# Performance work log

Measured on AMD Instinct MI355X. Metric: run time of the kernel, lower is better.

## Reference

```python
import jax, jax.numpy as jnp
import numpy as np

N_CODES = 1024
DIM = 64
COMMITMENT = 0.25


def setup_inputs() -> dict:
    key = jax.random.key(0)
    k1, k2 = jax.random.split(key)
    z = jax.random.normal(k1, (32, DIM, 64, 64), dtype=jnp.float32)
    # nn.Embedding weight initialized uniform(-1/n_codes, 1/n_codes)
    codebook = jax.random.uniform(
        k2, (N_CODES, DIM), dtype=jnp.float32,
        minval=-1.0 / N_CODES, maxval=1.0 / N_CODES)
    return {"z": z, "codebook": codebook}


def reference(z, codebook):
    B, C, H, W = z.shape
    # (B,C,H,W) -> (B*H*W, C)
    z_flat = jnp.transpose(z, (0, 2, 3, 1)).reshape(-1, C)
    # squared L2 distances via expansion: |z|^2 + |e|^2 - 2 z.e
    dists = (
        jnp.sum(z_flat ** 2, axis=1, keepdims=True)
        + jnp.sum(codebook ** 2, axis=1)
        - 2.0 * z_flat @ codebook.T
    )  # [N, n_codes]
    indices = jnp.argmin(dists, axis=1)  # [N]
    z_q = jnp.transpose(codebook[indices].reshape(B, H, W, C), (0, 3, 1, 2))
    commit_loss = jnp.mean((jax.lax.stop_gradient(z_q) - z) ** 2)
    codebook_loss = jnp.mean((z_q - jax.lax.stop_gradient(z)) ** 2)
    vq_loss = codebook_loss + COMMITMENT * commit_loss
    z_q_st = z + jax.lax.stop_gradient(z_q - z)  # straight-through
    return (z_q_st, vq_loss)
```

## Files before the change

kernel.cpp:

```cpp
#include <hip/hip_runtime.h>


constexpr int DIM    = 64;
constexpr int NCODES = 1024;
constexpr int HWSZ   = 4096;
constexpr int NPOS   = 131072;
constexpr int BLOCK  = 1024;
constexpr int PPB    = 256;
constexpr int GRID   = NPOS / PPB;

typedef float    f32x4  __attribute__((ext_vector_type(4)));
typedef float    f32x2  __attribute__((ext_vector_type(2)));
typedef unsigned uint2v __attribute__((ext_vector_type(2)));
typedef unsigned uint4v __attribute__((ext_vector_type(4)));

__global__ __launch_bounds__(256) void vq_prep(const float* __restrict__ cb,
                                               float* __restrict__ cinitT,
                                               unsigned* __restrict__ cbq) {
    int j = blockIdx.x * 256 + threadIdx.x;
    const float4* src = (const float4*)(cb + (size_t)j * DIM);
    unsigned words[16];
    float nq = 0.f;
#pragma unroll
    for (int g8 = 0; g8 < 8; g8++) {
        float4 v0 = src[g8 * 2], v1 = src[g8 * 2 + 1];
        int lo = 0, hi = 0;
        lo = __builtin_amdgcn_cvt_pk_fp8_f32(v0.x * 512.f, v0.y * 512.f, lo, 0);
        lo = __builtin_amdgcn_cvt_pk_fp8_f32(v0.z * 512.f, v0.w * 512.f, lo, 1);
        hi = __builtin_amdgcn_cvt_pk_fp8_f32(v1.x * 512.f, v1.y * 512.f, hi, 0);
        hi = __builtin_amdgcn_cvt_pk_fp8_f32(v1.z * 512.f, v1.w * 512.f, hi, 1);
        words[g8 * 2] = (unsigned)lo; words[g8 * 2 + 1] = (unsigned)hi;
#pragma unroll
        for (int m = 0; m < 2; m++) {
            int wv = m ? hi : lo;
            f32x2 d0 = __builtin_amdgcn_cvt_pk_f32_fp8(wv, 0);
            f32x2 d1 = __builtin_amdgcn_cvt_pk_f32_fp8(wv, 1);
            nq += d0[0] * d0[0] + d0[1] * d0[1] + d1[0] * d1[0] + d1[1] * d1[1];
        }
    }
#pragma unroll
    for (int u = 0; u < 4; u++) {
        int us = u ^ (j & 3);
        uint4v t = {words[2 * u], words[2 * u + 1],
                    words[2 * u + 8], words[2 * u + 9]};
        *(uint4v*)(cbq + (size_t)j * 16 + us * 4) = t;
    }
    cinitT[(j & 15) * 64 + (j >> 4)] = 8.f - nq * (1.f / 1024.f);
}

__global__ __launch_bounds__(BLOCK, 8) void vq_main(const float* __restrict__ z,
                                                    const float* __restrict__ cinitT,
                                                    const unsigned* __restrict__ cbq,
                                                    float* __restrict__ out,
                                                    float* __restrict__ wsblk) {
    __shared__ __align__(16) unsigned char cb_lds[NCODES * DIM];
    __shared__ int   bj_lds[PPB];
    __shared__ float ls_lds[BLOCK / 64];

    const int tid  = threadIdx.x;
    const int w    = tid >> 6;
    const int lane = tid & 63;
    const int q    = lane >> 4;
    const int r    = lane & 15;
    const int p0   = blockIdx.x * PPB;
    const int b    = p0 >> 12;
    const int hwb  = p0 & 4095;

#pragma unroll
    for (int it = 0; it < (NCODES * DIM) / (BLOCK * 16); it++) {
        int off = (it * BLOCK + tid) * 16;
        __builtin_amdgcn_global_load_lds(
            (const __attribute__((address_space(1))) void*)((const char*)cbq + off),
            (__attribute__((address_space(3))) void*)(cb_lds + off), 16, 0, 0);
    }

    long  afrag[2];
    float zsq;
    {
        const float* zb = z + (size_t)b * DIM * HWSZ + hwb + w * 16 + r;
        float sq = 0.f;
#pragma unroll
        for (int h = 0; h < 2; h++) {
            float v[8];
#pragma unroll
            for (int i = 0; i < 8; i++) {
                v[i] = zb[(size_t)(h * 32 + q * 8 + i) * HWSZ];
                sq = fmaf(v[i], v[i], sq);
            }
            int lo = 0, hi = 0;
            lo = __builtin_amdgcn_cvt_pk_fp8_f32(v[0], v[1], lo, 0);
            lo = __builtin_amdgcn_cvt_pk_fp8_f32(v[2], v[3], lo, 1);
            hi = __builtin_amdgcn_cvt_pk_fp8_f32(v[4], v[5], hi, 0);
            hi = __builtin_amdgcn_cvt_pk_fp8_f32(v[6], v[7], hi, 1);
            uint2v u = {(unsigned)lo, (unsigned)hi};
            afrag[h] = __builtin_bit_cast(long, u);
        }
        sq += __shfl_xor(sq, 16, 64);
        sq += __shfl_xor(sq, 32, 64);
        zsq = sq;
    }

    __syncthreads();

    const int bbase = r * 64 + ((q ^ (r & 3)) * 16);

    float best[4];
#pragma unroll
    for (int g = 0; g < 4; g++) best[g] = 0.f;
    float tmp[4];

    uint4v Bp[2];
    Bp[0] = *(const uint4v*)&cb_lds[0 * 1024 + bbase];
    Bp[1] = *(const uint4v*)&cb_lds[1 * 1024 + bbase];
    float4 ci[2];
    ci[0] = *(const float4*)(cinitT + r * 64 + 0);
    ci[1] = *(const float4*)(cinitT + r * 64 + 4);

#pragma unroll
    for (int G = 0; G < 16; G++) {
#pragma unroll
        for (int e = 0; e < 4; e++) {
            const int jt   = G * 4 + e;
            const int slot = jt & 1;
            const int row  = jt * 16;
            const float cin = ci[G & 1][e];
            const unsigned inv_j = (unsigned)(1023 - row);
            uint2v blo = {Bp[slot][0], Bp[slot][1]};
            uint2v bhi = {Bp[slot][2], Bp[slot][3]};
            f32x4 c0 = {cin, cin, cin, cin};
            f32x4 acc = __builtin_amdgcn_mfma_f32_16x16x32_fp8_fp8(
                afrag[0], __builtin_bit_cast(long, blo), c0, 0, 0, 0);
            acc = __builtin_amdgcn_mfma_f32_16x16x32_fp8_fp8(
                afrag[1], __builtin_bit_cast(long, bhi), acc, 0, 0, 0);
#pragma unroll
            for (int g = 0; g < 4; g++) {
                unsigned bits = (__float_as_uint(acc[g]) & ~1023u)
                              | (inv_j - (unsigned)r);
                float pf = __uint_as_float(bits);
                if ((jt & 1) == 0) {
                    tmp[g] = pf;
                } else {
                    best[g] = fmaxf(fmaxf(best[g], tmp[g]), pf);
                }
            }
            Bp[slot] = *(const uint4v*)&cb_lds[(((jt + 2) & 63) * 1024) + bbase];
        }
        ci[G & 1] = *(const float4*)(cinitT + r * 64 + (((G + 2) & 15) * 4));
    }

    unsigned bestu[4];
#pragma unroll
    for (int g = 0; g < 4; g++) {
        unsigned v = __float_as_uint(best[g]);
#pragma unroll
        for (int off = 1; off < 16; off <<= 1) {
            unsigned v2 = __shfl_xor((int)v, off, 64);
            v = v > v2 ? v : v2;
        }
        bestu[g] = v;
    }

    float lsum = 0.f;
    if (q == (r >> 2)) {
        int g = r & 3;
        unsigned v = bestu[0];
        v = (g == 1) ? bestu[1] : v;
        v = (g == 2) ? bestu[2] : v;
        v = (g == 3) ? bestu[3] : v;
        bj_lds[w * 16 + r] = 1023 - (int)(v & 1023u);
        lsum = zsq + (8.f - __uint_as_float(v)) * (1.f / 256.f);
    }
#pragma unroll
    for (int off = 32; off > 0; off >>= 1) lsum += __shfl_down(lsum, off, 64);
    if (lane == 0) ls_lds[w] = lsum;
    __syncthreads();
    if (tid == 0) {
        float s = 0.f;
#pragma unroll
        for (int i = 0; i < BLOCK / 64; i++) s += ls_lds[i];
        wsblk[blockIdx.x] = s;
    }

    int posi = tid & 255;
    int u    = tid >> 8;
    int myj  = bj_lds[posi];
    int us   = u ^ (myj & 3);
    uint4v t = *(const uint4v*)&cb_lds[(size_t)myj * 64 + us * 16];
    float* ob = out + (size_t)b * DIM * HWSZ + hwb + posi;
#pragma unroll
    for (int m = 0; m < 2; m++) {
        int cbase = (m == 0) ? (8 * u) : (32 + 8 * u);
#pragma unroll
        for (int wd = 0; wd < 2; wd++) {
            int word = (int)t[m * 2 + wd];
            f32x2 d0 = __builtin_amdgcn_cvt_pk_f32_fp8(word, 0);
            f32x2 d1 = __builtin_amdgcn_cvt_pk_f32_fp8(word, 1);
            ob[(size_t)(cbase + wd * 4 + 0) * HWSZ] = d0[0] * (1.f / 512.f);
            ob[(size_t)(cbase + wd * 4 + 1) * HWSZ] = d0[1] * (1.f / 512.f);
            ob[(size_t)(cbase + wd * 4 + 2) * HWSZ] = d1[0] * (1.f / 512.f);
            ob[(size_t)(cbase + wd * 4 + 3) * HWSZ] = d1[1] * (1.f / 512.f);
        }
    }
}

__global__ void vq_fin(const float* __restrict__ wsblk, float* __restrict__ out_loss) {
    int t = threadIdx.x;
    float s = 0.f;
#pragma unroll
    for (int k = 0; k < GRID / 64; k++) s += wsblk[t + k * 64];
#pragma unroll
    for (int off = 32; off > 0; off >>= 1) s += __shfl_down(s, off, 64);
    if (t == 0) out_loss[0] = 1.25f * s / (float)((size_t)NPOS * DIM);
}

extern "C" void kernel_launch(void* const* d_in, const int* in_sizes, int n_in,
                              void* d_out, int out_size, void* d_ws, size_t ws_size,
                              hipStream_t stream) {
    const float* z  = (const float*)d_in[0];
    const float* cb = (const float*)d_in[1];
    float* out = (float*)d_out;

    float*    cinitT = (float*)d_ws;
    unsigned* cbq    = (unsigned*)((char*)d_ws + 4096);
    float*    wsblk  = (float*)((char*)d_ws + 4096 + 65536);

    vq_prep<<<NCODES / 256, 256, 0, stream>>>(cb, cinitT, cbq);
    vq_main<<<GRID, BLOCK, 0, stream>>>(z, cinitT, cbq, out, wsblk);
    vq_fin<<<1, 64, 0, stream>>>(wsblk, out + (size_t)NPOS * DIM);
}
```

Measured before the change: 106.3 us.

## Split z quantization into a separate pre-pass kernel writing packed fp8 fragments

Moves the fp32 z read, fp8 packing and |z|^2 partial sums out of the main search kernel into a new full-grid vq_quant kernel, which also absorbs the codebook prep on its first four blocks. The main kernel then loads one 16-byte packed fragment per lane instead of 16 strided fp32 loads, so the LDS-occupying, MFMA-bound kernel spends less time waiting on global memory. In exchange it adds a full extra launch and an 8 MB intermediate write and read. It also relies on codebook prep finishing before vq_main, which stream ordering guarantees.

After: 109.0 us. +2.5%, slower.

```diff
diff --git a/kernel.cpp b/kernel.cpp
--- a/kernel.cpp
+++ b/kernel.cpp
@@ -14,49 +14,13 @@
 typedef unsigned uint2v __attribute__((ext_vector_type(2)));
 typedef unsigned uint4v __attribute__((ext_vector_type(4)));
 
-__global__ __launch_bounds__(256) void vq_prep(const float* __restrict__ cb,
-                                               float* __restrict__ cinitT,
-                                               unsigned* __restrict__ cbq) {
-    int j = blockIdx.x * 256 + threadIdx.x;
-    const float4* src = (const float4*)(cb + (size_t)j * DIM);
-    unsigned words[16];
-    float nq = 0.f;
-#pragma unroll
-    for (int g8 = 0; g8 < 8; g8++) {
-        float4 v0 = src[g8 * 2], v1 = src[g8 * 2 + 1];
-        int lo = 0, hi = 0;
-        lo = __builtin_amdgcn_cvt_pk_fp8_f32(v0.x * 512.f, v0.y * 512.f, lo, 0);
-        lo = __builtin_amdgcn_cvt_pk_fp8_f32(v0.z * 512.f, v0.w * 512.f, lo, 1);
-        hi = __builtin_amdgcn_cvt_pk_fp8_f32(v1.x * 512.f, v1.y * 512.f, hi, 0);
-        hi = __builtin_amdgcn_cvt_pk_fp8_f32(v1.z * 512.f, v1.w * 512.f, hi, 1);
-        words[g8 * 2] = (unsigned)lo; words[g8 * 2 + 1] = (unsigned)hi;
-#pragma unroll
-        for (int m = 0; m < 2; m++) {
-            int wv = m ? hi : lo;
-            f32x2 d0 = __builtin_amdgcn_cvt_pk_f32_fp8(wv, 0);
-            f32x2 d1 = __builtin_amdgcn_cvt_pk_f32_fp8(wv, 1);
-            nq += d0[0] * d0[0] + d0[1] * d0[1] + d1[0] * d1[0] + d1[1] * d1[1];
-        }
-    }
-#pragma unroll
-    for (int u = 0; u < 4; u++) {
-        int us = u ^ (j & 3);
-        uint4v t = {words[2 * u], words[2 * u + 1],
-                    words[2 * u + 8], words[2 * u + 9]};
-        *(uint4v*)(cbq + (size_t)j * 16 + us * 4) = t;
-    }
-    cinitT[(j & 15) * 64 + (j >> 4)] = 8.f - nq * (1.f / 1024.f);
-}
-
-__global__ __launch_bounds__(BLOCK, 8) void vq_main(const float* __restrict__ z,
-                                                    const float* __restrict__ cinitT,
-                                                    const unsigned* __restrict__ cbq,
-                                                    float* __restrict__ out,
-                                                    float* __restrict__ wsblk) {
-    __shared__ __align__(16) unsigned char cb_lds[NCODES * DIM];
-    __shared__ int   bj_lds[PPB];
+__global__ __launch_bounds__(BLOCK, 8) void vq_quant(const float* __restrict__ z,
+                                                     const float* __restrict__ cb,
+                                                     float* __restrict__ cinitT,
+                                                     unsigned* __restrict__ cbq,
+                                                     unsigned* __restrict__ zq,
+                                                     float* __restrict__ zs) {
     __shared__ float ls_lds[BLOCK / 64];
-
     const int tid  = threadIdx.x;
     const int w    = tid >> 6;
     const int lane = tid & 63;
@@ -66,6 +30,89 @@
     const int b    = p0 >> 12;
     const int hwb  = p0 & 4095;
 
+    const float* zb = z + (size_t)b * DIM * HWSZ + hwb + w * 16 + r;
+    float sq = 0.f;
+    unsigned wd[4];
+#pragma unroll
+    for (int h = 0; h < 2; h++) {
+        float v[8];
+#pragma unroll
+        for (int i = 0; i < 8; i++) {
+            v[i] = zb[(size_t)(h * 32 + q * 8 + i) * HWSZ];
+            sq = fmaf(v[i], v[i], sq);
+        }
+        int lo = 0, hi = 0;
+        lo = __builtin_amdgcn_cvt_pk_fp8_f32(v[0], v[1], lo, 0);
+        lo = __builtin_amdgcn_cvt_pk_fp8_f32(v[2], v[3], lo, 1);
+        hi = __builtin_amdgcn_cvt_pk_fp8_f32(v[4], v[5], hi, 0);
+        hi = __builtin_amdgcn_cvt_pk_fp8_f32(v[6], v[7], hi, 1);
+        wd[h * 2] = (unsigned)lo; wd[h * 2 + 1] = (unsigned)hi;
+    }
+    uint4v av = {wd[0], wd[1], wd[2], wd[3]};
+    *(uint4v*)(zq + ((size_t)(blockIdx.x * 16 + w) * 64 + lane) * 4) = av;
+
+#pragma unroll
+    for (int off = 32; off > 0; off >>= 1) sq += __shfl_down(sq, off, 64);
+    if (lane == 0) ls_lds[w] = sq;
+    __syncthreads();
+    if (tid == 0) {
+        float s = 0.f;
+#pragma unroll
+        for (int i = 0; i < BLOCK / 64; i++) s += ls_lds[i];
+        zs[blockIdx.x] = s;
+    }
+
+    if (blockIdx.x < 4 && tid < 256) {
+        int j = blockIdx.x * 256 + tid;
+        const float4* src = (const float4*)(cb + (size_t)j * DIM);
+        unsigned words[16];
+        float nq = 0.f;
+#pragma unroll
+        for (int g8 = 0; g8 < 8; g8++) {
+            float4 v0 = src[g8 * 2], v1 = src[g8 * 2 + 1];
+            int lo = 0, hi = 0;
+            lo = __builtin_amdgcn_cvt_pk_fp8_f32(v0.x * 512.f, v0.y * 512.f, lo, 0);
+            lo = __builtin_amdgcn_cvt_pk_fp8_f32(v0.z * 512.f, v0.w * 512.f, lo, 1);
+            hi = __builtin_amdgcn_cvt_pk_fp8_f32(v1.x * 512.f, v1.y * 512.f, hi, 0);
+            hi = __builtin_amdgcn_cvt_pk_fp8_f32(v1.z * 512.f, v1.w * 512.f, hi, 1);
+            words[g8 * 2] = (unsigned)lo; words[g8 * 2 + 1] = (unsigned)hi;
+#pragma unroll
+            for (int m = 0; m < 2; m++) {
+                int wv = m ? hi : lo;
+                f32x2 d0 = __builtin_amdgcn_cvt_pk_f32_fp8(wv, 0);
+                f32x2 d1 = __builtin_amdgcn_cvt_pk_f32_fp8(wv, 1);
+                nq += d0[0] * d0[0] + d0[1] * d0[1] + d1[0] * d1[0] + d1[1] * d1[1];
+            }
+        }
+#pragma unroll
+        for (int u = 0; u < 4; u++) {
+            int us = u ^ (j & 3);
+            uint4v t = {words[2 * u], words[2 * u + 1],
+                        words[2 * u + 8], words[2 * u + 9]};
+            *(uint4v*)(cbq + (size_t)j * 16 + us * 4) = t;
+        }
+        cinitT[(j & 15) * 64 + (j >> 4)] = 8.f - nq * (1.f / 1024.f);
+    }
+}
+
+__global__ __launch_bounds__(BLOCK, 8) void vq_main(const unsigned* __restrict__ zq,
+                                                    const float* __restrict__ cinitT,
+                                                    const unsigned* __restrict__ cbq,
+                                                    float* __restrict__ out,
+                                                    float* __restrict__ sc) {
+    __shared__ __align__(16) unsigned char cb_lds[NCODES * DIM];
+    __shared__ int   bj_lds[PPB];
+    __shared__ float ls_lds[BLOCK / 64];
+
+    const int tid  = threadIdx.x;
+    const int w    = tid >> 6;
+    const int lane = tid & 63;
+    const int q    = lane >> 4;
+    const int r    = lane & 15;
+    const int p0   = blockIdx.x * PPB;
+    const int b    = p0 >> 12;
+    const int hwb  = p0 & 4095;
+
 #pragma unroll
     for (int it = 0; it < (NCODES * DIM) / (BLOCK * 16); it++) {
         int off = (it * BLOCK + tid) * 16;
@@ -74,31 +121,10 @@
             (__attribute__((address_space(3))) void*)(cb_lds + off), 16, 0, 0);
     }
 
-    long  afrag[2];
-    float zsq;
-    {
-        const float* zb = z + (size_t)b * DIM * HWSZ + hwb + w * 16 + r;
-        float sq = 0.f;
-#pragma unroll
-        for (int h = 0; h < 2; h++) {
-            float v[8];
-#pragma unroll
-            for (int i = 0; i < 8; i++) {
-                v[i] = zb[(size_t)(h * 32 + q * 8 + i) * HWSZ];
-                sq = fmaf(v[i], v[i], sq);
-            }
-            int lo = 0, hi = 0;
-            lo = __builtin_amdgcn_cvt_pk_fp8_f32(v[0], v[1], lo, 0);
-            lo = __builtin_amdgcn_cvt_pk_fp8_f32(v[2], v[3], lo, 1);
-            hi = __builtin_amdgcn_cvt_pk_fp8_f32(v[4], v[5], hi, 0);
-            hi = __builtin_amdgcn_cvt_pk_fp8_f32(v[6], v[7], hi, 1);
-            uint2v u = {(unsigned)lo, (unsigned)hi};
-            afrag[h] = __builtin_bit_cast(long, u);
-        }
-        sq += __shfl_xor(sq, 16, 64);
-        sq += __shfl_xor(sq, 32, 64);
-        zsq = sq;
-    }
+    uint4v av = *(const uint4v*)(zq + ((size_t)(blockIdx.x * 16 + w) * 64 + lane) * 4);
+    uint2v a0 = {av[0], av[1]}, a1 = {av[2], av[3]};
+    const long afrag0 = __builtin_bit_cast(long, a0);
+    const long afrag1 = __builtin_bit_cast(long, a1);
 
     __syncthreads();
 
@@ -129,9 +155,9 @@
             uint2v bhi = {Bp[slot][2], Bp[slot][3]};
             f32x4 c0 = {cin, cin, cin, cin};
             f32x4 acc = __builtin_amdgcn_mfma_f32_16x16x32_fp8_fp8(
-                afrag[0], __builtin_bit_cast(long, blo), c0, 0, 0, 0);
+                afrag0, __builtin_bit_cast(long, blo), c0, 0, 0, 0);
             acc = __builtin_amdgcn_mfma_f32_16x16x32_fp8_fp8(
-                afrag[1], __builtin_bit_cast(long, bhi), acc, 0, 0, 0);
+                afrag1, __builtin_bit_cast(long, bhi), acc, 0, 0, 0);
 #pragma unroll
             for (int g = 0; g < 4; g++) {
                 unsigned bits = (__float_as_uint(acc[g]) & ~1023u)
@@ -168,7 +194,7 @@
         v = (g == 2) ? bestu[2] : v;
         v = (g == 3) ? bestu[3] : v;
         bj_lds[w * 16 + r] = 1023 - (int)(v & 1023u);
-        lsum = zsq + (8.f - __uint_as_float(v)) * (1.f / 256.f);
+        lsum = (8.f - __uint_as_float(v)) * (1.f / 256.f);
     }
 #pragma unroll
     for (int off = 32; off > 0; off >>= 1) lsum += __shfl_down(lsum, off, 64);
@@ -178,7 +204,7 @@
         float s = 0.f;
 #pragma unroll
         for (int i = 0; i < BLOCK / 64; i++) s += ls_lds[i];
-        wsblk[blockIdx.x] = s;
+        sc[blockIdx.x] = s;
     }
 
     int posi = tid & 255;
@@ -191,23 +217,24 @@
     for (int m = 0; m < 2; m++) {
         int cbase = (m == 0) ? (8 * u) : (32 + 8 * u);
 #pragma unroll
-        for (int wd = 0; wd < 2; wd++) {
-            int word = (int)t[m * 2 + wd];
+        for (int wdx = 0; wdx < 2; wdx++) {
+            int word = (int)t[m * 2 + wdx];
             f32x2 d0 = __builtin_amdgcn_cvt_pk_f32_fp8(word, 0);
             f32x2 d1 = __builtin_amdgcn_cvt_pk_f32_fp8(word, 1);
-            ob[(size_t)(cbase + wd * 4 + 0) * HWSZ] = d0[0] * (1.f / 512.f);
-            ob[(size_t)(cbase + wd * 4 + 1) * HWSZ] = d0[1] * (1.f / 512.f);
-            ob[(size_t)(cbase + wd * 4 + 2) * HWSZ] = d1[0] * (1.f / 512.f);
-            ob[(size_t)(cbase + wd * 4 + 3) * HWSZ] = d1[1] * (1.f / 512.f);
-        }
-    }
-}
-
-__global__ void vq_fin(const float* __restrict__ wsblk, float* __restrict__ out_loss) {
+            ob[(size_t)(cbase + wdx * 4 + 0) * HWSZ] = d0[0] * (1.f / 512.f);
+            ob[(size_t)(cbase + wdx * 4 + 1) * HWSZ] = d0[1] * (1.f / 512.f);
+            ob[(size_t)(cbase + wdx * 4 + 2) * HWSZ] = d1[0] * (1.f / 512.f);
+            ob[(size_t)(cbase + wdx * 4 + 3) * HWSZ] = d1[1] * (1.f / 512.f);
+        }
+    }
+}
+
+__global__ void vq_fin(const float* __restrict__ zs, const float* __restrict__ sc,
+                       float* __restrict__ out_loss) {
     int t = threadIdx.x;
     float s = 0.f;
 #pragma unroll
-    for (int k = 0; k < GRID / 64; k++) s += wsblk[t + k * 64];
+    for (int k = 0; k < GRID / 64; k++) s += zs[t + k * 64] + sc[t + k * 64];
 #pragma unroll
     for (int off = 32; off > 0; off >>= 1) s += __shfl_down(s, off, 64);
     if (t == 0) out_loss[0] = 1.25f * s / (float)((size_t)NPOS * DIM);
@@ -222,9 +249,11 @@
 
     float*    cinitT = (float*)d_ws;
     unsigned* cbq    = (unsigned*)((char*)d_ws + 4096);
-    float*    wsblk  = (float*)((char*)d_ws + 4096 + 65536);
-
-    vq_prep<<<NCODES / 256, 256, 0, stream>>>(cb, cinitT, cbq);
-    vq_main<<<GRID, BLOCK, 0, stream>>>(z, cinitT, cbq, out, wsblk);
-    vq_fin<<<1, 64, 0, stream>>>(wsblk, out + (size_t)NPOS * DIM);
-}
+    unsigned* zq     = (unsigned*)((char*)d_ws + 4096 + 65536);
+    float*    zs     = (float*)((char*)d_ws + 4096 + 65536 + 8388608);
+    float*    sc     = (float*)((char*)d_ws + 4096 + 65536 + 8388608 + 2048);
+
+    vq_quant<<<GRID, BLOCK, 0, stream>>>(z, cb, cinitT, cbq, zq, zs);
+    vq_main<<<GRID, BLOCK, 0, stream>>>(zq, cinitT, cbq, out, sc);
+    vq_fin<<<1, 64, 0, stream>>>(zs, sc, out + (size_t)NPOS * DIM);
+}
```
